# Kernel optimization log

Measured on AMD Instinct MI355X. Metric: run time of the kernel, lower is better.

Reference implementation:

```python
import jax, jax.numpy as jnp
import numpy as np

EMBED_DIM = 768
N_HEADS = 12
HEAD_DIM = EMBED_DIM // N_HEADS


def setup_inputs() -> dict:
    key = jax.random.key(0)
    ks = jax.random.split(key, 5)
    B, T, C = 2, 4096, EMBED_DIM
    x = jax.random.normal(ks[0], (B, T, C), dtype=jnp.float32)
    # nn.Linear default init scale ~ 1/sqrt(fan_in); use small-scale normals
    s = 1.0 / np.sqrt(C)
    W_qkv = jax.random.normal(ks[1], (C, 3 * C), dtype=jnp.float32) * s
    b_qkv = jax.random.normal(ks[2], (3 * C,), dtype=jnp.float32) * s
    W_proj = jax.random.normal(ks[3], (C, C), dtype=jnp.float32) * s
    b_proj = jax.random.normal(ks[4], (C,), dtype=jnp.float32) * s
    return {"x": x, "W_qkv": W_qkv, "b_qkv": b_qkv, "W_proj": W_proj, "b_proj": b_proj}


def reference(x, W_qkv, b_qkv, W_proj, b_proj):
    B, T, C = x.shape
    H, D = N_HEADS, HEAD_DIM
    qkv = x @ W_qkv + b_qkv                      # [B,T,3C]
    q, k, v = jnp.split(qkv, 3, axis=2)
    # [B,T,C] -> [B,H,T,D]
    q = q.reshape(B, T, H, D).transpose(0, 2, 1, 3)
    k = k.reshape(B, T, H, D).transpose(0, 2, 1, 3)
    v = v.reshape(B, T, H, D).transpose(0, 2, 1, 3)
    scale = 1.0 / jnp.sqrt(jnp.float32(D)).astype(x.dtype)
    attn = jnp.einsum('bhtd,bhsd->bhts', q, k) * scale   # [B,H,T,T]
    causal = jnp.tril(jnp.ones((T, T), dtype=bool))
    attn = jnp.where(causal, attn, jnp.float32(-jnp.inf).astype(attn.dtype))
    attn = jax.nn.softmax(attn, axis=-1)
    # dropout p=0.0 -> identity
    out = jnp.einsum('bhts,bhsd->bhtd', attn, v)          # [B,H,T,D]
    out = out.transpose(0, 2, 1, 3).reshape(B, T, C)
    return out @ W_proj + b_proj
```

## Files before the change

### kernel.cpp

```cpp
#include <hip/hip_runtime.h>
#include <math.h>

#define T_SEQ 4096
#define CDIM  768
#define NH    12
#define HD    64
#define BATCH 2
#define MROWS (BATCH * T_SEQ)
#define N3C   (3 * CDIM)
#define HEADS_TOTAL (BATCH * NH)
#define QKV_ELEMS   ((size_t)HEADS_TOTAL * T_SEQ * HD)

#define QSCALE 0.18033688011112042f
#define SSHIFT -12.0f

typedef __bf16 bf16x8 __attribute__((ext_vector_type(8)));
typedef __bf16 bf16x4 __attribute__((ext_vector_type(4)));
typedef __bf16 bf16x2 __attribute__((ext_vector_type(2)));
typedef float  f32x4  __attribute__((ext_vector_type(4)));
typedef short  s16x4  __attribute__((ext_vector_type(4)));

union b4u { bf16x4 h; s16x4 s; };
__device__ __forceinline__ s16x4 as_s16(bf16x4 v) { b4u u; u.h = v; return u.s; }

typedef __attribute__((address_space(1))) const void as1_cvoid;
typedef __attribute__((address_space(3))) void as3_void;

__device__ __forceinline__ void gl16(const void* g, void* l) {
  __builtin_amdgcn_global_load_lds((as1_cvoid*)g, (as3_void*)l, 16, 0, 0);
}

__global__ __launch_bounds__(256) void cast_x_kernel(
    const float* __restrict__ x, __bf16* __restrict__ xb) {
  int i = (blockIdx.x * 256 + threadIdx.x) * 8;
  float4 a = *(const float4*)&x[i];
  float4 b = *(const float4*)&x[i + 4];
  bf16x8 o;
  o[0] = (__bf16)a.x; o[1] = (__bf16)a.y; o[2] = (__bf16)a.z; o[3] = (__bf16)a.w;
  o[4] = (__bf16)b.x; o[5] = (__bf16)b.y; o[6] = (__bf16)b.z; o[7] = (__bf16)b.w;
  *(bf16x8*)&xb[i] = o;
}

__global__ __launch_bounds__(256) void tcast_kernel(
    const float* __restrict__ W, __bf16* __restrict__ Wt, int K, int N) {
  __shared__ float tile[64][65];
  const int t  = threadIdx.x;
  const int k0 = blockIdx.y * 64, n0 = blockIdx.x * 64;
  const int r  = t >> 4, c4 = (t & 15) << 2;
#pragma unroll
  for (int i = 0; i < 4; ++i) {
    float4 v = *(const float4*)&W[(size_t)(k0 + r + i * 16) * N + n0 + c4];
    tile[r + i * 16][c4 + 0] = v.x; tile[r + i * 16][c4 + 1] = v.y;
    tile[r + i * 16][c4 + 2] = v.z; tile[r + i * 16][c4 + 3] = v.w;
  }
  __syncthreads();
#pragma unroll
  for (int i = 0; i < 4; ++i) {
    int nr = r + i * 16;
    bf16x4 o;
    o[0] = (__bf16)tile[c4 + 0][nr]; o[1] = (__bf16)tile[c4 + 1][nr];
    o[2] = (__bf16)tile[c4 + 2][nr]; o[3] = (__bf16)tile[c4 + 3][nr];
    *(bf16x4*)&Wt[(size_t)(n0 + nr) * K + k0 + c4] = o;
  }
}

__device__ __forceinline__ void mm_loop(const __bf16* __restrict__ A,
                                        const __bf16* __restrict__ Bt,
                                        int m0, int n0, __bf16* smem,
                                        f32x4 acc[4][4]) {
  const int t = threadIdx.x, wv = t >> 6, lane = t & 63;
  const int g2 = lane >> 4, c = lane & 15;
  __bf16* At = smem;
  __bf16* Bs = smem + 4096;
  const int ch0 = wv * 64 + lane;
  const int ch1 = 256 + ch0;
  const __bf16* gA0 = A  + (size_t)(m0 + (ch0 >> 2)) * CDIM + ((ch0 & 3) << 3);
  const __bf16* gA1 = A  + (size_t)(m0 + (ch1 >> 2)) * CDIM + ((ch1 & 3) << 3);
  const __bf16* gB0 = Bt + (size_t)(n0 + (ch0 >> 2)) * CDIM + ((ch0 & 3) << 3);
  const __bf16* gB1 = Bt + (size_t)(n0 + (ch1 >> 2)) * CDIM + ((ch1 & 3) << 3);
  __bf16* lA0 = At + (size_t)(wv * 64) * 8;
  __bf16* lA1 = At + (size_t)(256 + wv * 64) * 8;
  __bf16* lB0 = Bs + (size_t)(wv * 64) * 8;
  __bf16* lB1 = Bs + (size_t)(256 + wv * 64) * 8;
  const int mw = (wv & 1) << 6, nw = (wv >> 1) << 6;

  for (int kk = 0; kk < CDIM / 32; ++kk) {
    __syncthreads();
    gl16(gA0, lA0); gl16(gA1, lA1);
    gl16(gB0, lB0); gl16(gB1, lB1);
    gA0 += 32; gA1 += 32; gB0 += 32; gB1 += 32;
    __syncthreads();
    bf16x8 af[4], bfr[4];
#pragma unroll
    for (int mq = 0; mq < 4; ++mq)
      af[mq] = *(const bf16x8*)&At[(size_t)(mw + mq * 16 + c) * 32 + (g2 << 3)];
#pragma unroll
    for (int nq = 0; nq < 4; ++nq)
      bfr[nq] = *(const bf16x8*)&Bs[(size_t)(nw + nq * 16 + c) * 32 + (g2 << 3)];
#pragma unroll
    for (int mq = 0; mq < 4; ++mq)
#pragma unroll
      for (int nq = 0; nq < 4; ++nq)
        acc[mq][nq] = __builtin_amdgcn_mfma_f32_16x16x32_bf16(
            af[mq], bfr[nq], acc[mq][nq], 0, 0, 0);
  }
  __syncthreads();
}

__global__ __launch_bounds__(256) void qkv_mm_kernel(
    const __bf16* __restrict__ xb, const __bf16* __restrict__ Wt,
    const float* __restrict__ bias, __bf16* __restrict__ Qw,
    __bf16* __restrict__ Kw, __bf16* __restrict__ Vtw) {
  __shared__ __align__(16) __bf16 smem[18432];
  f32x4 acc[4][4];
#pragma unroll
  for (int i = 0; i < 4; ++i)
#pragma unroll
    for (int j = 0; j < 4; ++j) acc[i][j] = (f32x4){0.f, 0.f, 0.f, 0.f};

  const int m0 = blockIdx.y * 128, n0 = blockIdx.x * 128;
  mm_loop(xb, Wt, m0, n0, smem, acc);

  const int t = threadIdx.x, wv = t >> 6, lane = t & 63;
  const int g2 = lane >> 4, c = lane & 15;
  const int sel = n0 / CDIM;
  const int nn0 = n0 - sel * CDIM;
  const int h   = (nn0 >> 6) + (wv >> 1);
  const int mbase = m0 + ((wv & 1) << 6);
  const int b = mbase >> 12, tp0 = mbase & 4095;
  const int bh = b * NH + h;
  __bf16* Ep = smem + wv * 4608;
  float bcol[4];
#pragma unroll
  for (int nq = 0; nq < 4; ++nq)
    bcol[nq] = bias[n0 + ((wv >> 1) << 6) + nq * 16 + c];

  const int r8 = lane >> 3, c8 = (lane & 7) << 3;
  if (sel < 2) {
    const float scl = (sel == 0) ? QSCALE : 1.0f;
#pragma unroll
    for (int mq = 0; mq < 4; ++mq)
#pragma unroll
      for (int nq = 0; nq < 4; ++nq)
#pragma unroll
        for (int r = 0; r < 4; ++r)
          Ep[(size_t)(mq * 16 + (g2 << 2) + r) * 72 + nq * 16 + c] =
              (__bf16)((acc[mq][nq][r] + bcol[nq]) * scl);
    asm volatile("s_waitcnt lgkmcnt(0)" ::: "memory");
    __bf16* dst = (sel == 0) ? Qw : Kw;
#pragma unroll
    for (int p = 0; p < 8; ++p) {
      int row = p * 8 + r8;
      bf16x8 v = *(const bf16x8*)&Ep[(size_t)row * 72 + c8];
      *(bf16x8*)&dst[((size_t)bh * T_SEQ + tp0 + row) * HD + c8] = v;
    }
  } else {
#pragma unroll
    for (int mq = 0; mq < 4; ++mq)
#pragma unroll
      for (int nq = 0; nq < 4; ++nq)
#pragma unroll
        for (int r = 0; r < 4; ++r)
          Ep[(size_t)(nq * 16 + c) * 72 + mq * 16 + (g2 << 2) + r] =
              (__bf16)(acc[mq][nq][r] + bcol[nq]);
    asm volatile("s_waitcnt lgkmcnt(0)" ::: "memory");
#pragma unroll
    for (int p = 0; p < 8; ++p) {
      int d = p * 8 + r8;
      bf16x8 v = *(const bf16x8*)&Ep[(size_t)d * 72 + c8];
      *(bf16x8*)&Vtw[((size_t)bh * HD + d) * T_SEQ + tp0 + c8] = v;
    }
  }
}

__device__ __forceinline__ void stage_tile(const __bf16* gk, const __bf16* gv,
                                           __bf16* ldsK, __bf16* ldsV) {
  gl16(gk,              ldsK);
  gl16(gk + 8 * HD,     ldsK + 8 * 64);
  gl16(gv,              ldsV);
  gl16(gv + 8 * T_SEQ,  ldsV + 8 * 64);
}

__device__ __forceinline__ void attn_tile(
    const __bf16* __restrict__ Qb, const __bf16* __restrict__ Kb,
    const __bf16* __restrict__ Vb, __bf16* __restrict__ O,
    int b, int hh, int qt, int wv, int lane, int g2, int c,
    __bf16 (*KT)[64][64], __bf16 (*VT)[64][64]) {
  const int qw = qt * 64 + wv * 16;

  bf16x8 qf0 = *(const bf16x8*)&Qb[(size_t)(qw + c) * HD +      (g2 << 3)];
  bf16x8 qf1 = *(const bf16x8*)&Qb[(size_t)(qw + c) * HD + 32 + (g2 << 3)];

  f32x4 ot[4];
#pragma unroll
  for (int dt = 0; dt < 4; ++dt) ot[dt] = (f32x4){0.f, 0.f, 0.f, 0.f};
  f32x4 lacc = (f32x4){0.f, 0.f, 0.f, 0.f};

  const int rr = lane >> 3;
  const int lc = ((lane & 7) ^ rr) << 3;
  const __bf16* gk = Kb + (size_t)(wv * 16 + rr) * HD    + lc;
  const __bf16* gv = Vb + (size_t)(wv * 16 + rr) * T_SEQ + lc;

  stage_tile(gk, gv, &KT[0][wv * 16][0], &VT[0][wv * 16][0]);
  gk += 64 * HD; gv += 64;
  __syncthreads();

  const int swz  = (c & 7) << 3;
  const int qloc = (wv << 4) + c;
  const f32x4 SINIT = (f32x4){SSHIFT, SSHIFT, SSHIFT, SSHIFT};

#pragma unroll 1
  for (int kt = 0; kt <= qt; ++kt) {
    const int cur = kt & 1;
    if (kt < qt) {
      stage_tile(gk, gv, &KT[cur ^ 1][wv * 16][0], &VT[cur ^ 1][wv * 16][0]);
      gk += 64 * HD; gv += 64;
    }

    f32x4 S[4];
#pragma unroll
    for (int st = 0; st < 4; ++st) {
      bf16x8 kfa = *(const bf16x8*)&KT[cur][st * 16 + c][(g2 << 3) ^ swz];
      bf16x8 kfb = *(const bf16x8*)&KT[cur][st * 16 + c][((4 + g2) << 3) ^ swz];
      S[st] = __builtin_amdgcn_mfma_f32_16x16x32_bf16(kfa, qf0, SINIT, 0, 0, 0);
      S[st] = __builtin_amdgcn_mfma_f32_16x16x32_bf16(kfb, qf1, S[st], 0, 0, 0);
    }

    if (kt == qt) {
#pragma unroll
      for (int st = 0; st < 4; ++st)
#pragma unroll
        for (int r = 0; r < 4; ++r)
          if ((st << 4) + (g2 << 2) + r > qloc) S[st][r] = -INFINITY;
    }

    s16x4 pf[4];
#pragma unroll
    for (int st = 0; st < 4; ++st) {
      bf16x4 ph;
#pragma unroll
      for (int r = 0; r < 4; ++r) {
        float pl = __builtin_amdgcn_exp2f(S[st][r]);
        lacc[r] += pl;
        ph[r] = (__bf16)pl;
      }
      pf[st] = as_s16(ph);
    }

#pragma unroll
    for (int dt = 0; dt < 4; ++dt) {
#pragma unroll
      for (int st = 0; st < 4; ++st) {
        bf16x4 vh = *(const bf16x4*)&VT[cur][dt * 16 + c]
                                       [((st << 4) + (g2 << 2)) ^ swz];
        ot[dt] = __builtin_amdgcn_mfma_f32_16x16x16bf16_1k(as_s16(vh), pf[st],
                                                           ot[dt], 0, 0, 0);
      }
    }
    __syncthreads();
  }

  float l = lacc[0] + lacc[1] + lacc[2] + lacc[3];
  l += __shfl_xor(l, 16);
  l += __shfl_xor(l, 32);
  const float inv = 1.f / l;
  __bf16* orow = O + ((size_t)(b * T_SEQ + qw + c)) * CDIM + hh * HD;
#pragma unroll
  for (int dt = 0; dt < 4; ++dt) {
    bf16x4 v;
    v[0] = (__bf16)(ot[dt][0] * inv); v[1] = (__bf16)(ot[dt][1] * inv);
    v[2] = (__bf16)(ot[dt][2] * inv); v[3] = (__bf16)(ot[dt][3] * inv);
    *(bf16x4*)&orow[dt * 16 + (g2 << 2)] = v;
  }
}

__global__ __launch_bounds__(256) void attn_kernel(
    const __bf16* __restrict__ Q, const __bf16* __restrict__ K,
    const __bf16* __restrict__ Vt, __bf16* __restrict__ O) {
  __shared__ __align__(16) __bf16 KT[2][64][64];
  __shared__ __align__(16) __bf16 VT[2][64][64];

  const int t    = threadIdx.x;
  const int wv   = t >> 6;
  const int lane = t & 63;
  const int g2   = lane >> 4;
  const int c    = lane & 15;
  const int bh   = blockIdx.x;
  const int p    = (int)blockIdx.y;

  const __bf16* Qb = Q  + (size_t)bh * T_SEQ * HD;
  const __bf16* Kb = K  + (size_t)bh * T_SEQ * HD;
  const __bf16* Vb = Vt + (size_t)bh * HD * T_SEQ;
  const int b = bh / NH, hh = bh % NH;

  attn_tile(Qb, Kb, Vb, O, b, hh, p,      wv, lane, g2, c, KT, VT);
  attn_tile(Qb, Kb, Vb, O, b, hh, 63 - p, wv, lane, g2, c, KT, VT);
}

__global__ __launch_bounds__(256) void proj_mm_kernel(
    const __bf16* __restrict__ Ob, const __bf16* __restrict__ Wt,
    const float* __restrict__ bias, float* __restrict__ out) {
  __shared__ __align__(16) __bf16 smem[8192];
  f32x4 acc[4][4];
#pragma unroll
  for (int i = 0; i < 4; ++i)
#pragma unroll
    for (int j = 0; j < 4; ++j) acc[i][j] = (f32x4){0.f, 0.f, 0.f, 0.f};

  const int m0 = blockIdx.y * 128, n0 = blockIdx.x * 128;
  mm_loop(Ob, Wt, m0, n0, smem, acc);

  const int t = threadIdx.x, wv = t >> 6, lane = t & 63;
  const int g2 = lane >> 4, c = lane & 15;
  const int mb = m0 + ((wv & 1) << 6), nb = n0 + ((wv >> 1) << 6);
  float bcol[4];
#pragma unroll
  for (int nq = 0; nq < 4; ++nq) bcol[nq] = bias[nb + nq * 16 + c];
#pragma unroll
  for (int mq = 0; mq < 4; ++mq)
#pragma unroll
    for (int nq = 0; nq < 4; ++nq)
#pragma unroll
      for (int r = 0; r < 4; ++r)
        out[(size_t)(mb + mq * 16 + (g2 << 2) + r) * CDIM + nb + nq * 16 + c] =
            acc[mq][nq][r] + bcol[nq];
}

extern "C" void kernel_launch(void* const* d_in, const int* in_sizes, int n_in,
                              void* d_out, int out_size, void* d_ws, size_t ws_size,
                              hipStream_t stream) {
  (void)in_sizes; (void)n_in; (void)out_size; (void)ws_size;
  const float* x      = (const float*)d_in[0];
  const float* W_qkv  = (const float*)d_in[1];
  const float* b_qkv  = (const float*)d_in[2];
  const float* W_proj = (const float*)d_in[3];
  const float* b_proj = (const float*)d_in[4];
  float* out = (float*)d_out;

  __bf16* Qw     = (__bf16*)d_ws;
  __bf16* Kw     = Qw  + QKV_ELEMS;
  __bf16* Vtw    = Kw  + QKV_ELEMS;
  __bf16* Ob     = Vtw + QKV_ELEMS;
  __bf16* xb     = Ob  + QKV_ELEMS;
  __bf16* Wqkvt  = xb  + QKV_ELEMS;
  __bf16* Wprojt = Wqkvt + (size_t)CDIM * N3C;

  cast_x_kernel<<<MROWS * CDIM / 2048, 256, 0, stream>>>(x, xb);
  tcast_kernel<<<dim3(N3C / 64, CDIM / 64), 256, 0, stream>>>(
      W_qkv, Wqkvt, CDIM, N3C);
  tcast_kernel<<<dim3(CDIM / 64, CDIM / 64), 256, 0, stream>>>(
      W_proj, Wprojt, CDIM, CDIM);

  qkv_mm_kernel<<<dim3(N3C / 128, MROWS / 128), 256, 0, stream>>>(
      xb, Wqkvt, b_qkv, Qw, Kw, Vtw);

  attn_kernel<<<dim3(HEADS_TOTAL, 32), 256, 0, stream>>>(Qw, Kw, Vtw, Ob);

  proj_mm_kernel<<<dim3(CDIM / 128, MROWS / 128), 256, 0, stream>>>(
      Ob, Wprojt, b_proj, out);
}
```

Measured before the change: 249.4 us.

## Double GEMM K-step to 64 and compute softmax row sums via MFMA

The shared GEMM main loop now stages a 64-wide K slice per iteration as two 32-wide panels, which halves the number of barrier pairs and global-to-LDS rounds. The projection kernel's LDS buffer doubles to fit this. In attention, the per-lane exp accumulation and the cross-lane shuffle reduction are replaced by an extra MFMA against a ones vector that yields the row sums directly. The row sums are now taken from bf16-rounded probabilities, adding four MFMAs per key tile, and the larger LDS footprint may reduce occupancy.

New measurement: 254.0 us. No clear change (+1.9%).

```diff
diff --git a/kernel.cpp b/kernel.cpp
--- a/kernel.cpp
+++ b/kernel.cpp
@@ -71,38 +71,48 @@
   const int t = threadIdx.x, wv = t >> 6, lane = t & 63;
   const int g2 = lane >> 4, c = lane & 15;
   __bf16* At = smem;
-  __bf16* Bs = smem + 4096;
-  const int ch0 = wv * 64 + lane;
-  const int ch1 = 256 + ch0;
-  const __bf16* gA0 = A  + (size_t)(m0 + (ch0 >> 2)) * CDIM + ((ch0 & 3) << 3);
-  const __bf16* gA1 = A  + (size_t)(m0 + (ch1 >> 2)) * CDIM + ((ch1 & 3) << 3);
-  const __bf16* gB0 = Bt + (size_t)(n0 + (ch0 >> 2)) * CDIM + ((ch0 & 3) << 3);
-  const __bf16* gB1 = Bt + (size_t)(n0 + (ch1 >> 2)) * CDIM + ((ch1 & 3) << 3);
-  __bf16* lA0 = At + (size_t)(wv * 64) * 8;
-  __bf16* lA1 = At + (size_t)(256 + wv * 64) * 8;
-  __bf16* lB0 = Bs + (size_t)(wv * 64) * 8;
-  __bf16* lB1 = Bs + (size_t)(256 + wv * 64) * 8;
+  __bf16* Bs = smem + 8192;
+
+  const __bf16 *gA[4], *gB[4];
+  __bf16 *lA[4], *lB[4];
+#pragma unroll
+  for (int i = 0; i < 4; ++i) {
+    const int d   = i * 256 + wv * 64 + lane;
+    const int row = (d >> 2) & 127;
+    const int pan = d >> 9;
+    const int c4  = d & 3;
+    gA[i] = A  + (size_t)(m0 + row) * CDIM + pan * 32 + c4 * 8;
+    gB[i] = Bt + (size_t)(n0 + row) * CDIM + pan * 32 + c4 * 8;
+    lA[i] = At + (size_t)(i * 256 + wv * 64) * 8;
+    lB[i] = Bs + (size_t)(i * 256 + wv * 64) * 8;
+  }
   const int mw = (wv & 1) << 6, nw = (wv >> 1) << 6;
 
-  for (int kk = 0; kk < CDIM / 32; ++kk) {
+  for (int kk = 0; kk < CDIM / 64; ++kk) {
     __syncthreads();
-    gl16(gA0, lA0); gl16(gA1, lA1);
-    gl16(gB0, lB0); gl16(gB1, lB1);
-    gA0 += 32; gA1 += 32; gB0 += 32; gB1 += 32;
+#pragma unroll
+    for (int i = 0; i < 4; ++i) { gl16(gA[i], lA[i]); gl16(gB[i], lB[i]); }
+#pragma unroll
+    for (int i = 0; i < 4; ++i) { gA[i] += 64; gB[i] += 64; }
     __syncthreads();
-    bf16x8 af[4], bfr[4];
-#pragma unroll
-    for (int mq = 0; mq < 4; ++mq)
-      af[mq] = *(const bf16x8*)&At[(size_t)(mw + mq * 16 + c) * 32 + (g2 << 3)];
-#pragma unroll
-    for (int nq = 0; nq < 4; ++nq)
-      bfr[nq] = *(const bf16x8*)&Bs[(size_t)(nw + nq * 16 + c) * 32 + (g2 << 3)];
-#pragma unroll
-    for (int mq = 0; mq < 4; ++mq)
+#pragma unroll
+    for (int s = 0; s < 2; ++s) {
+      bf16x8 af[4], bfr[4];
+#pragma unroll
+      for (int mq = 0; mq < 4; ++mq)
+        af[mq] = *(const bf16x8*)&At[s * 4096 +
+                                     (size_t)(mw + mq * 16 + c) * 32 + (g2 << 3)];
 #pragma unroll
       for (int nq = 0; nq < 4; ++nq)
-        acc[mq][nq] = __builtin_amdgcn_mfma_f32_16x16x32_bf16(
-            af[mq], bfr[nq], acc[mq][nq], 0, 0, 0);
+        bfr[nq] = *(const bf16x8*)&Bs[s * 4096 +
+                                      (size_t)(nw + nq * 16 + c) * 32 + (g2 << 3)];
+#pragma unroll
+      for (int mq = 0; mq < 4; ++mq)
+#pragma unroll
+        for (int nq = 0; nq < 4; ++nq)
+          acc[mq][nq] = __builtin_amdgcn_mfma_f32_16x16x32_bf16(
+              af[mq], bfr[nq], acc[mq][nq], 0, 0, 0);
+    }
   }
   __syncthreads();
 }
@@ -194,7 +204,10 @@
   f32x4 ot[4];
 #pragma unroll
   for (int dt = 0; dt < 4; ++dt) ot[dt] = (f32x4){0.f, 0.f, 0.f, 0.f};
-  f32x4 lacc = (f32x4){0.f, 0.f, 0.f, 0.f};
+  f32x4 lt = (f32x4){0.f, 0.f, 0.f, 0.f};
+
+  const bf16x4 onev = {(__bf16)1.f, (__bf16)1.f, (__bf16)1.f, (__bf16)1.f};
+  const s16x4 ones = as_s16(onev);
 
   const int rr = lane >> 3;
   const int lc = ((lane & 7) ^ rr) << 3;
@@ -241,7 +254,6 @@
 #pragma unroll
       for (int r = 0; r < 4; ++r) {
         float pl = __builtin_amdgcn_exp2f(S[st][r]);
-        lacc[r] += pl;
         ph[r] = (__bf16)pl;
       }
       pf[st] = as_s16(ph);
@@ -257,13 +269,14 @@
                                                            ot[dt], 0, 0, 0);
       }
     }
+#pragma unroll
+    for (int st = 0; st < 4; ++st)
+      lt = __builtin_amdgcn_mfma_f32_16x16x16bf16_1k(ones, pf[st], lt, 0, 0, 0);
+
     __syncthreads();
   }
 
-  float l = lacc[0] + lacc[1] + lacc[2] + lacc[3];
-  l += __shfl_xor(l, 16);
-  l += __shfl_xor(l, 32);
-  const float inv = 1.f / l;
+  const float inv = 1.f / lt[0];
   __bf16* orow = O + ((size_t)(b * T_SEQ + qw + c)) * CDIM + hh * HD;
 #pragma unroll
   for (int dt = 0; dt < 4; ++dt) {
@@ -300,7 +313,7 @@
 __global__ __launch_bounds__(256) void proj_mm_kernel(
     const __bf16* __restrict__ Ob, const __bf16* __restrict__ Wt,
     const float* __restrict__ bias, float* __restrict__ out) {
-  __shared__ __align__(16) __bf16 smem[8192];
+  __shared__ __align__(16) __bf16 smem[16384];
   f32x4 acc[4][4];
 #pragma unroll
   for (int i = 0; i < 4; ++i)
```

## Load V fragments directly from global and compute row sums via MFMA

Applied to the files above, without the earlier changes.

V tiles are no longer staged through shared memory. Each wave reads its V MFMA operand fragments straight from global memory (L2) into registers at the start of each key tile, which halves LDS usage and drops the V LDS reads. The softmax denominator is now built with an extra MFMA against a ones vector instead of scalar adds and cross-lane shuffles. The cost is that all four waves redundantly fetch the same V data from global or cache with 8-byte loads, which adds load latency to the critical path and raises register pressure.

Result: slower. 509.8 us (+104.4%).

```diff
diff --git a/kernel.cpp b/kernel.cpp
--- a/kernel.cpp
+++ b/kernel.cpp
@@ -173,19 +173,16 @@
   }
 }
 
-__device__ __forceinline__ void stage_tile(const __bf16* gk, const __bf16* gv,
-                                           __bf16* ldsK, __bf16* ldsV) {
-  gl16(gk,              ldsK);
-  gl16(gk + 8 * HD,     ldsK + 8 * 64);
-  gl16(gv,              ldsV);
-  gl16(gv + 8 * T_SEQ,  ldsV + 8 * 64);
+__device__ __forceinline__ void stage_tile(const __bf16* gk, __bf16* ldsK) {
+  gl16(gk,          ldsK);
+  gl16(gk + 8 * HD, ldsK + 8 * 64);
 }
 
 __device__ __forceinline__ void attn_tile(
     const __bf16* __restrict__ Qb, const __bf16* __restrict__ Kb,
     const __bf16* __restrict__ Vb, __bf16* __restrict__ O,
     int b, int hh, int qt, int wv, int lane, int g2, int c,
-    __bf16 (*KT)[64][64], __bf16 (*VT)[64][64]) {
+    __bf16 (*KT)[64][64]) {
   const int qw = qt * 64 + wv * 16;
 
   bf16x8 qf0 = *(const bf16x8*)&Qb[(size_t)(qw + c) * HD +      (g2 << 3)];
@@ -194,15 +191,22 @@
   f32x4 ot[4];
 #pragma unroll
   for (int dt = 0; dt < 4; ++dt) ot[dt] = (f32x4){0.f, 0.f, 0.f, 0.f};
-  f32x4 lacc = (f32x4){0.f, 0.f, 0.f, 0.f};
+  f32x4 lt = (f32x4){0.f, 0.f, 0.f, 0.f};
+
+  const bf16x4 onev = {(__bf16)1.f, (__bf16)1.f, (__bf16)1.f, (__bf16)1.f};
+  const s16x4 ones = as_s16(onev);
 
   const int rr = lane >> 3;
   const int lc = ((lane & 7) ^ rr) << 3;
-  const __bf16* gk = Kb + (size_t)(wv * 16 + rr) * HD    + lc;
-  const __bf16* gv = Vb + (size_t)(wv * 16 + rr) * T_SEQ + lc;
-
-  stage_tile(gk, gv, &KT[0][wv * 16][0], &VT[0][wv * 16][0]);
-  gk += 64 * HD; gv += 64;
+  const __bf16* gk = Kb + (size_t)(wv * 16 + rr) * HD + lc;
+
+  const __bf16* vp0 = Vb + (size_t)( 0 + c) * T_SEQ + (g2 << 2);
+  const __bf16* vp1 = Vb + (size_t)(16 + c) * T_SEQ + (g2 << 2);
+  const __bf16* vp2 = Vb + (size_t)(32 + c) * T_SEQ + (g2 << 2);
+  const __bf16* vp3 = Vb + (size_t)(48 + c) * T_SEQ + (g2 << 2);
+
+  stage_tile(gk, &KT[0][wv * 16][0]);
+  gk += 64 * HD;
   __syncthreads();
 
   const int swz  = (c & 7) << 3;
@@ -212,9 +216,20 @@
 #pragma unroll 1
   for (int kt = 0; kt <= qt; ++kt) {
     const int cur = kt & 1;
+
+    bf16x4 vfr[4][4];
+#pragma unroll
+    for (int st = 0; st < 4; ++st) {
+      vfr[0][st] = *(const bf16x4*)(vp0 + st * 16);
+      vfr[1][st] = *(const bf16x4*)(vp1 + st * 16);
+      vfr[2][st] = *(const bf16x4*)(vp2 + st * 16);
+      vfr[3][st] = *(const bf16x4*)(vp3 + st * 16);
+    }
+    vp0 += 64; vp1 += 64; vp2 += 64; vp3 += 64;
+
     if (kt < qt) {
-      stage_tile(gk, gv, &KT[cur ^ 1][wv * 16][0], &VT[cur ^ 1][wv * 16][0]);
-      gk += 64 * HD; gv += 64;
+      stage_tile(gk, &KT[cur ^ 1][wv * 16][0]);
+      gk += 64 * HD;
     }
 
     f32x4 S[4];
@@ -241,7 +256,6 @@
 #pragma unroll
       for (int r = 0; r < 4; ++r) {
         float pl = __builtin_amdgcn_exp2f(S[st][r]);
-        lacc[r] += pl;
         ph[r] = (__bf16)pl;
       }
       pf[st] = as_s16(ph);
@@ -251,19 +265,18 @@
     for (int dt = 0; dt < 4; ++dt) {
 #pragma unroll
       for (int st = 0; st < 4; ++st) {
-        bf16x4 vh = *(const bf16x4*)&VT[cur][dt * 16 + c]
-                                       [((st << 4) + (g2 << 2)) ^ swz];
-        ot[dt] = __builtin_amdgcn_mfma_f32_16x16x16bf16_1k(as_s16(vh), pf[st],
-                                                           ot[dt], 0, 0, 0);
+        ot[dt] = __builtin_amdgcn_mfma_f32_16x16x16bf16_1k(
+            as_s16(vfr[dt][st]), pf[st], ot[dt], 0, 0, 0);
       }
     }
+#pragma unroll
+    for (int st = 0; st < 4; ++st)
+      lt = __builtin_amdgcn_mfma_f32_16x16x16bf16_1k(ones, pf[st], lt, 0, 0, 0);
+
     __syncthreads();
   }
 
-  float l = lacc[0] + lacc[1] + lacc[2] + lacc[3];
-  l += __shfl_xor(l, 16);
-  l += __shfl_xor(l, 32);
-  const float inv = 1.f / l;
+  const float inv = 1.f / lt[0];
   __bf16* orow = O + ((size_t)(b * T_SEQ + qw + c)) * CDIM + hh * HD;
 #pragma unroll
   for (int dt = 0; dt < 4; ++dt) {
@@ -278,7 +291,6 @@
     const __bf16* __restrict__ Q, const __bf16* __restrict__ K,
     const __bf16* __restrict__ Vt, __bf16* __restrict__ O) {
   __shared__ __align__(16) __bf16 KT[2][64][64];
-  __shared__ __align__(16) __bf16 VT[2][64][64];
 
   const int t    = threadIdx.x;
   const int wv   = t >> 6;
@@ -293,8 +305,8 @@
   const __bf16* Vb = Vt + (size_t)bh * HD * T_SEQ;
   const int b = bh / NH, hh = bh % NH;
 
-  attn_tile(Qb, Kb, Vb, O, b, hh, p,      wv, lane, g2, c, KT, VT);
-  attn_tile(Qb, Kb, Vb, O, b, hh, 63 - p, wv, lane, g2, c, KT, VT);
+  attn_tile(Qb, Kb, Vb, O, b, hh, p,      wv, lane, g2, c, KT);
+  attn_tile(Qb, Kb, Vb, O, b, hh, 63 - p, wv, lane, g2, c, KT);
 }
 
 __global__ __launch_bounds__(256) void proj_mm_kernel(
```

## Halve attention block to two waves, each handling two query sub-tiles

Applied to the files above, without the earlier changes.

The attention kernel now launches 128 threads (2 waves) per block instead of 256, and each wave processes two 16-row query sub-tiles. Each K fragment loaded from LDS is therefore reused for two QK^T MFMAs and each V fragment for two PV MFMAs, and each wave stages 32 K/V rows per tile. The softmax row sum moves from per-lane VALU adds plus cross-lane shuffles to an MFMA against a ones vector. This raises register pressure and cuts waves per block, which risks lower latency hiding in exchange for fewer LDS reads per MFMA.

Result: slower. 263.7 us (+5.8%).

```diff
diff --git a/kernel.cpp b/kernel.cpp
--- a/kernel.cpp
+++ b/kernel.cpp
@@ -173,12 +173,16 @@
   }
 }
 
-__device__ __forceinline__ void stage_tile(const __bf16* gk, const __bf16* gv,
-                                           __bf16* ldsK, __bf16* ldsV) {
-  gl16(gk,              ldsK);
-  gl16(gk + 8 * HD,     ldsK + 8 * 64);
-  gl16(gv,              ldsV);
-  gl16(gv + 8 * T_SEQ,  ldsV + 8 * 64);
+__device__ __forceinline__ void stage64(const __bf16* gk, const __bf16* gv,
+                                        __bf16* ldsK, __bf16* ldsV) {
+  gl16(gk,               ldsK);
+  gl16(gk + 8  * HD,     ldsK + 8  * 64);
+  gl16(gk + 16 * HD,     ldsK + 16 * 64);
+  gl16(gk + 24 * HD,     ldsK + 24 * 64);
+  gl16(gv,               ldsV);
+  gl16(gv + 8  * T_SEQ,  ldsV + 8  * 64);
+  gl16(gv + 16 * T_SEQ,  ldsV + 16 * 64);
+  gl16(gv + 24 * T_SEQ,  ldsV + 24 * 64);
 }
 
 __device__ __forceinline__ void attn_tile(
@@ -186,65 +190,81 @@
     const __bf16* __restrict__ Vb, __bf16* __restrict__ O,
     int b, int hh, int qt, int wv, int lane, int g2, int c,
     __bf16 (*KT)[64][64], __bf16 (*VT)[64][64]) {
-  const int qw = qt * 64 + wv * 16;
-
-  bf16x8 qf0 = *(const bf16x8*)&Qb[(size_t)(qw + c) * HD +      (g2 << 3)];
-  bf16x8 qf1 = *(const bf16x8*)&Qb[(size_t)(qw + c) * HD + 32 + (g2 << 3)];
-
-  f32x4 ot[4];
-#pragma unroll
-  for (int dt = 0; dt < 4; ++dt) ot[dt] = (f32x4){0.f, 0.f, 0.f, 0.f};
-  f32x4 lacc = (f32x4){0.f, 0.f, 0.f, 0.f};
+  const int q0 = qt * 64 + wv * 16;
+  const int q1 = q0 + 32;
+
+  bf16x8 qa0 = *(const bf16x8*)&Qb[(size_t)(q0 + c) * HD +      (g2 << 3)];
+  bf16x8 qa1 = *(const bf16x8*)&Qb[(size_t)(q0 + c) * HD + 32 + (g2 << 3)];
+  bf16x8 qb0 = *(const bf16x8*)&Qb[(size_t)(q1 + c) * HD +      (g2 << 3)];
+  bf16x8 qb1 = *(const bf16x8*)&Qb[(size_t)(q1 + c) * HD + 32 + (g2 << 3)];
+
+  f32x4 oa[4], ob[4];
+#pragma unroll
+  for (int dt = 0; dt < 4; ++dt) {
+    oa[dt] = (f32x4){0.f, 0.f, 0.f, 0.f};
+    ob[dt] = (f32x4){0.f, 0.f, 0.f, 0.f};
+  }
+  f32x4 la = (f32x4){0.f, 0.f, 0.f, 0.f};
+  f32x4 lb = (f32x4){0.f, 0.f, 0.f, 0.f};
+
+  const bf16x4 onev = {(__bf16)1.f, (__bf16)1.f, (__bf16)1.f, (__bf16)1.f};
+  const s16x4 ones = as_s16(onev);
 
   const int rr = lane >> 3;
   const int lc = ((lane & 7) ^ rr) << 3;
-  const __bf16* gk = Kb + (size_t)(wv * 16 + rr) * HD    + lc;
-  const __bf16* gv = Vb + (size_t)(wv * 16 + rr) * T_SEQ + lc;
-
-  stage_tile(gk, gv, &KT[0][wv * 16][0], &VT[0][wv * 16][0]);
+  const __bf16* gk = Kb + (size_t)(wv * 32 + rr) * HD    + lc;
+  const __bf16* gv = Vb + (size_t)(wv * 32 + rr) * T_SEQ + lc;
+
+  stage64(gk, gv, &KT[0][wv * 32][0], &VT[0][wv * 32][0]);
   gk += 64 * HD; gv += 64;
   __syncthreads();
 
-  const int swz  = (c & 7) << 3;
-  const int qloc = (wv << 4) + c;
+  const int swz   = (c & 7) << 3;
+  const int qloc0 = (wv << 4) + c;
+  const int qloc1 = 32 + (wv << 4) + c;
   const f32x4 SINIT = (f32x4){SSHIFT, SSHIFT, SSHIFT, SSHIFT};
 
 #pragma unroll 1
   for (int kt = 0; kt <= qt; ++kt) {
     const int cur = kt & 1;
     if (kt < qt) {
-      stage_tile(gk, gv, &KT[cur ^ 1][wv * 16][0], &VT[cur ^ 1][wv * 16][0]);
+      stage64(gk, gv, &KT[cur ^ 1][wv * 32][0], &VT[cur ^ 1][wv * 32][0]);
       gk += 64 * HD; gv += 64;
     }
 
-    f32x4 S[4];
+    f32x4 Sa[4], Sb[4];
 #pragma unroll
     for (int st = 0; st < 4; ++st) {
       bf16x8 kfa = *(const bf16x8*)&KT[cur][st * 16 + c][(g2 << 3) ^ swz];
       bf16x8 kfb = *(const bf16x8*)&KT[cur][st * 16 + c][((4 + g2) << 3) ^ swz];
-      S[st] = __builtin_amdgcn_mfma_f32_16x16x32_bf16(kfa, qf0, SINIT, 0, 0, 0);
-      S[st] = __builtin_amdgcn_mfma_f32_16x16x32_bf16(kfb, qf1, S[st], 0, 0, 0);
+      Sa[st] = __builtin_amdgcn_mfma_f32_16x16x32_bf16(kfa, qa0, SINIT, 0, 0, 0);
+      Sa[st] = __builtin_amdgcn_mfma_f32_16x16x32_bf16(kfb, qa1, Sa[st], 0, 0, 0);
+      Sb[st] = __builtin_amdgcn_mfma_f32_16x16x32_bf16(kfa, qb0, SINIT, 0, 0, 0);
+      Sb[st] = __builtin_amdgcn_mfma_f32_16x16x32_bf16(kfb, qb1, Sb[st], 0, 0, 0);
     }
 
     if (kt == qt) {
 #pragma unroll
       for (int st = 0; st < 4; ++st)
 #pragma unroll
-        for (int r = 0; r < 4; ++r)
-          if ((st << 4) + (g2 << 2) + r > qloc) S[st][r] = -INFINITY;
-    }
-
-    s16x4 pf[4];
+        for (int r = 0; r < 4; ++r) {
+          const int sl = (st << 4) + (g2 << 2) + r;
+          if (sl > qloc0) Sa[st][r] = -INFINITY;
+          if (sl > qloc1) Sb[st][r] = -INFINITY;
+        }
+    }
+
+    s16x4 pa[4], pb[4];
 #pragma unroll
     for (int st = 0; st < 4; ++st) {
-      bf16x4 ph;
+      bf16x4 pha, phb;
 #pragma unroll
       for (int r = 0; r < 4; ++r) {
-        float pl = __builtin_amdgcn_exp2f(S[st][r]);
-        lacc[r] += pl;
-        ph[r] = (__bf16)pl;
+        pha[r] = (__bf16)__builtin_amdgcn_exp2f(Sa[st][r]);
+        phb[r] = (__bf16)__builtin_amdgcn_exp2f(Sb[st][r]);
       }
-      pf[st] = as_s16(ph);
+      pa[st] = as_s16(pha);
+      pb[st] = as_s16(phb);
     }
 
 #pragma unroll
@@ -253,28 +273,45 @@
       for (int st = 0; st < 4; ++st) {
         bf16x4 vh = *(const bf16x4*)&VT[cur][dt * 16 + c]
                                        [((st << 4) + (g2 << 2)) ^ swz];
-        ot[dt] = __builtin_amdgcn_mfma_f32_16x16x16bf16_1k(as_s16(vh), pf[st],
-                                                           ot[dt], 0, 0, 0);
+        s16x4 vs = as_s16(vh);
+        oa[dt] = __builtin_amdgcn_mfma_f32_16x16x16bf16_1k(vs, pa[st], oa[dt], 0, 0, 0);
+        ob[dt] = __builtin_amdgcn_mfma_f32_16x16x16bf16_1k(vs, pb[st], ob[dt], 0, 0, 0);
       }
     }
+#pragma unroll
+    for (int st = 0; st < 4; ++st) {
+      la = __builtin_amdgcn_mfma_f32_16x16x16bf16_1k(ones, pa[st], la, 0, 0, 0);
+      lb = __builtin_amdgcn_mfma_f32_16x16x16bf16_1k(ones, pb[st], lb, 0, 0, 0);
+    }
+
     __syncthreads();
   }
 
-  float l = lacc[0] + lacc[1] + lacc[2] + lacc[3];
-  l += __shfl_xor(l, 16);
-  l += __shfl_xor(l, 32);
-  const float inv = 1.f / l;
-  __bf16* orow = O + ((size_t)(b * T_SEQ + qw + c)) * CDIM + hh * HD;
-#pragma unroll
-  for (int dt = 0; dt < 4; ++dt) {
-    bf16x4 v;
-    v[0] = (__bf16)(ot[dt][0] * inv); v[1] = (__bf16)(ot[dt][1] * inv);
-    v[2] = (__bf16)(ot[dt][2] * inv); v[3] = (__bf16)(ot[dt][3] * inv);
-    *(bf16x4*)&orow[dt * 16 + (g2 << 2)] = v;
-  }
-}
-
-__global__ __launch_bounds__(256) void attn_kernel(
+  {
+    const float inv = 1.f / la[0];
+    __bf16* orow = O + ((size_t)(b * T_SEQ + q0 + c)) * CDIM + hh * HD;
+#pragma unroll
+    for (int dt = 0; dt < 4; ++dt) {
+      bf16x4 v;
+      v[0] = (__bf16)(oa[dt][0] * inv); v[1] = (__bf16)(oa[dt][1] * inv);
+      v[2] = (__bf16)(oa[dt][2] * inv); v[3] = (__bf16)(oa[dt][3] * inv);
+      *(bf16x4*)&orow[dt * 16 + (g2 << 2)] = v;
+    }
+  }
+  {
+    const float inv = 1.f / lb[0];
+    __bf16* orow = O + ((size_t)(b * T_SEQ + q1 + c)) * CDIM + hh * HD;
+#pragma unroll
+    for (int dt = 0; dt < 4; ++dt) {
+      bf16x4 v;
+      v[0] = (__bf16)(ob[dt][0] * inv); v[1] = (__bf16)(ob[dt][1] * inv);
+      v[2] = (__bf16)(ob[dt][2] * inv); v[3] = (__bf16)(ob[dt][3] * inv);
+      *(bf16x4*)&orow[dt * 16 + (g2 << 2)] = v;
+    }
+  }
+}
+
+__global__ __launch_bounds__(128) void attn_kernel(
     const __bf16* __restrict__ Q, const __bf16* __restrict__ K,
     const __bf16* __restrict__ Vt, __bf16* __restrict__ O) {
   __shared__ __align__(16) __bf16 KT[2][64][64];
@@ -354,7 +391,7 @@
   qkv_mm_kernel<<<dim3(N3C / 128, MROWS / 128), 256, 0, stream>>>(
       xb, Wqkvt, b_qkv, Qw, Kw, Vtw);
 
-  attn_kernel<<<dim3(HEADS_TOTAL, 32), 256, 0, stream>>>(Qw, Kw, Vtw, Ob);
+  attn_kernel<<<dim3(HEADS_TOTAL, 32), 128, 0, stream>>>(Qw, Kw, Vtw, Ob);
 
   proj_mm_kernel<<<dim3(CDIM / 128, MROWS / 128), 256, 0, stream>>>(
       Ob, Wprojt, b_proj, out);
```
